# Kernel tuning notes

Measured on AMD Instinct MI355X. Metric: run time of the kernel, lower is better.

The kernel has to match this reference:

```python
import jax, jax.numpy as jnp
import numpy as np

B, S, L, H, E, V = 32, 48, 48, 1024, 1024, 32000


def setup_inputs() -> dict:
    key = jax.random.key(0)
    ks = jax.random.split(key, 16)
    s = 0.02
    return {
        "label": jax.random.randint(ks[0], (B, S), 0, V),
        "init_hidden": jax.random.normal(ks[1], (1, B, H), jnp.float32),
        "encoder_output": jax.random.normal(ks[2], (B, L, H), jnp.float32),
        "emb": jax.random.normal(ks[3], (V, E), jnp.float32) * s,
        "attn_W": jax.random.normal(ks[4], (2 * H, L), jnp.float32) * s,
        "attn_b": jnp.zeros((L,), jnp.float32),
        "comb_W": jax.random.normal(ks[5], (2 * H, H), jnp.float32) * s,
        "comb_b": jnp.zeros((H,), jnp.float32),
        "W_ih": jax.random.normal(ks[6], (E, 3 * H), jnp.float32) * s,
        "W_hh": jax.random.normal(ks[7], (H, 3 * H), jnp.float32) * s,
        "b_ih": jnp.zeros((3 * H,), jnp.float32),
        "b_hh": jnp.zeros((3 * H,), jnp.float32),
        "out_W": jax.random.normal(ks[8], (H, V), jnp.float32) * s,
        "out_b": jnp.zeros((V,), jnp.float32),
    }


def _decode(label, init_hidden, encoder_output, emb, attn_W, attn_b,
            comb_W, comb_b, W_ih, W_hh, b_ih, b_hh, out_W, out_b):
    # Teacher forcing (teaching_force_rate=1.0): inputs are relu(embedding(label[:, i]))
    xs = jax.nn.relu(emb[label])            # (B, S, E)
    xs = jnp.transpose(xs, (1, 0, 2))       # (S, B, E) for scan

    def step(h, xe):                        # h: (B,H), xe: (B,E)
        # Attention: Linear(cat(emb, hidden)) -> nn.Softmax() on a 3D (B,1,L)
        # tensor, which in torch defaults to dim=0 (the batch dim) -- replicated.
        sim = jnp.concatenate([xe, h], axis=-1) @ attn_W + attn_b   # (B, L)
        w = jax.nn.softmax(sim, axis=0)                             # over batch (faithful)
        ctx = jnp.einsum('bl,blh->bh', w, encoder_output)           # bmm
        g = jax.nn.relu(jnp.concatenate([ctx, xe], axis=-1) @ comb_W + comb_b)  # (B,H)
        # Single GRU step (torch gate order: r, z, n)
        gx = g @ W_ih + b_ih
        gh = h @ W_hh + b_hh
        xr, xz, xn = jnp.split(gx, 3, axis=-1)
        hr, hz, hn = jnp.split(gh, 3, axis=-1)
        r = jax.nn.sigmoid(xr + hr)
        z = jax.nn.sigmoid(xz + hz)
        n = jnp.tanh(xn + r * hn)
        h_new = (1.0 - z) * n + z * h
        out = jax.nn.log_softmax(h_new @ out_W + out_b, axis=-1)    # (B, V)
        return h_new, out

    _, outs = jax.lax.scan(step, init_hidden[0], xs)   # outs: (S, B, V)
    return jnp.transpose(outs, (1, 0, 2))              # (B, S, V)


def reference(label, init_hidden, encoder_output, emb, attn_W, attn_b,
              comb_W, comb_b, W_ih, W_hh, b_ih, b_hh, out_W, out_b):
    return _decode(label, init_hidden, encoder_output, emb, attn_W, attn_b,
                   comb_W, comb_b, W_ih, W_hh, b_ih, b_hh, out_W, out_b)
```

## Files before the change

### kernel.cpp

```cpp
#include <hip/hip_runtime.h>

#define NB 32
#define NS 48
#define NL 48
#define NH 1024
#define NE 1024
#define NV 32000
#define NR (NS*NB)
#define K3H 3072
#define RA_BLOCKS 64
#define RB_BLOCKS 128
#define RC_BLOCKS 64
#define NBLK_FULL (RA_BLOCKS + RB_BLOCKS + RC_BLOCKS)

typedef unsigned short u16;
typedef __bf16 bf16x8 __attribute__((ext_vector_type(8)));
typedef unsigned short ushort8 __attribute__((ext_vector_type(8)));
typedef float f32x4 __attribute__((ext_vector_type(4)));
typedef unsigned int uint4v __attribute__((ext_vector_type(4)));

__device__ __forceinline__ float bf2f(u16 x) {
    union { unsigned u; float f; } c; c.u = ((unsigned)x) << 16; return c.f;
}
__device__ __forceinline__ u16 f2bf(float f) {
// ... 29 lines not shown
    if ((prev & lineMask) == lineMask) {
        int p2 = __hip_atomic_fetch_add(superc, 1, __ATOMIC_RELAXED, __HIP_MEMORY_SCOPE_AGENT);
        if ((p2 & 7) == 7) {
#pragma unroll
            for (int i = 0; i < 24; ++i)
                asm volatile("global_store_dword %0, %1, off sc0 sc1"
                             :: "v"(bcast + i * 64), "v"(val) : "memory");
        }
    }
}

__global__ __launch_bounds__(256) void transpose_cast(const float* __restrict__ src, int K, int N,
                                                      char* __restrict__ dst, int bf16out) {
    __shared__ float tile[32][33];
    int k0 = blockIdx.y * 32, n0 = blockIdx.x * 32;
    int tx = threadIdx.x & 31, ty = threadIdx.x >> 5;
    for (int i = 0; i < 4; ++i) {
        int n = n0 + tx;
        float v = (n < N) ? src[(size_t)(k0 + ty + i*8) * N + n] : 0.f;
        tile[ty + i*8][tx] = v;
    }
    __syncthreads();
    for (int i = 0; i < 4; ++i) {
        int n = n0 + ty + i*8;
        int k = k0 + tx;
        if (n < N) {
            float v = tile[tx][ty + i*8];
            if (bf16out) ((u16*)dst)[(size_t)n * K + k] = f2bf(v);
            else         ((float*)dst)[(size_t)n * K + k] = v;
        }
    }
}

__global__ __launch_bounds__(256) void transpose_all(const float* __restrict__ Whh_, const float* __restrict__ Wih_,
                                                     const float* __restrict__ combW_, const float* __restrict__ attnW_,
                                                     u16* __restrict__ whht, u16* __restrict__ wiht,
                                                     u16* __restrict__ cw1t, u16* __restrict__ cw2t,
                                                     u16* __restrict__ aw2t, u16* __restrict__ aw1t) {
    __shared__ float tile[32][33];
    int bid = blockIdx.x;
    const float* src; u16* dst; int N, local;
    if (bid < 3072)      { src = Whh_;  dst = whht; N = 3072; local = bid; }
    else if (bid < 6144) { src = Wih_;  dst = wiht; N = 3072; local = bid - 3072; }
    else if (bid < 7168) { src = combW_; dst = cw1t; N = 1024; local = bid - 6144; }
    else if (bid < 8192) { src = combW_ + (size_t)NH * NH; dst = cw2t; N = 1024; local = bid - 7168; }
    else if (bid < 8256) { src = attnW_ + (size_t)NH * NL; dst = aw2t; N = 48; local = bid - 8192; }
    else                 { src = attnW_; dst = aw1t; N = 48; local = bid - 8256; }
    int tiles_x = (N + 31) >> 5;
    int n0 = (local % tiles_x) * 32, k0 = (local / tiles_x) * 32;
    int tx = threadIdx.x & 31, ty = threadIdx.x >> 5;
    for (int i = 0; i < 4; ++i) {
        int n = n0 + tx;
        float v = (n < N) ? src[(size_t)(k0 + ty + i*8) * N + n] : 0.f;
        tile[ty + i*8][tx] = v;
    }
    __syncthreads();
    for (int i = 0; i < 4; ++i) {
        int n = n0 + ty + i*8;
        int k = k0 + tx;
        if (n < N) dst[(size_t)n * 1024 + k] = f2bf(tile[tx][ty + i*8]);
    }
}

__global__ __launch_bounds__(256) void prep_inputs(const int* __restrict__ label, const float* __restrict__ emb,
                                                   const float* __restrict__ enc, const float* __restrict__ inith,
                                                   u16* __restrict__ xe, u16* __restrict__ encb, u16* __restrict__ hallx) {
    int blk = blockIdx.x, t = threadIdx.x;
    if (blk < NR) {
        int s = blk >> 5, b = blk & 31;
        int lab = label[b * NS + s];
        const float* src = emb + (size_t)lab * NE;
        u16* dst = xe + (size_t)blk * NE;
        for (int i = t; i < NE; i += 256) { float v = src[i]; dst[i] = f2bf(v > 0.f ? v : 0.f); }
    } else if (blk < 2 * NR) {
        int r = blk - NR;
        const float* src = enc + (size_t)r * NH;
        u16* dst = encb + (size_t)r * NH;
        for (int i = t; i < NH; i += 256) dst[i] = f2bf(src[i]);
    } else {
        int b = blk - 2 * NR;
        const float* src = inith + (size_t)b * NH;
        u16* dst = hallx + (size_t)b * NH;
        for (int i = t; i < NH; i += 256) dst[i] = f2bf(src[i]);
    }
}

__global__ __launch_bounds__(384) void simxe2_kernel(const u16* __restrict__ xe, const u16* __restrict__ aw1t,
                                                     const float* __restrict__ attnB, float* __restrict__ simxe) {
    int r = blockIdx.x, t = threadIdx.x;
    int l = t >> 3, part = t & 7;
    const u16* x = xe + (size_t)r * 1024 + part * 128;
    const u16* ww = aw1t + (size_t)l * 1024 + part * 128;
    float acc = 0.f;
#pragma unroll
    for (int k = 0; k < 128; k += 8) {
        ushort8 xv = *reinterpret_cast<const ushort8*>(x + k);
        ushort8 wv = *reinterpret_cast<const ushort8*>(ww + k);
#pragma unroll
        for (int u = 0; u < 8; ++u) acc += bf2f(xv[u]) * bf2f(wv[u]);
    }
    acc += __shfl_xor(acc, 1);
    acc += __shfl_xor(acc, 2);
    acc += __shfl_xor(acc, 4);
    if (part == 0) simxe[(size_t)r * NL + l] = acc + attnB[l];
}

template<int MODE>
__global__ __launch_bounds__(256) void gemm_bf16(const u16* __restrict__ A, const u16* __restrict__ Bt,
                                                 void* __restrict__ Cout, const float* __restrict__ bias, int N) {
    __shared__ u16 ldsA[128 * 64];
    __shared__ u16 ldsB[128 * 64];
    const int t = threadIdx.x;
    const int lane = t & 63, w = t >> 6;
    const int wm = w >> 1, wn = w & 1;
    const int m0 = blockIdx.x * 128, n0 = blockIdx.y * 128;
    f32x4 acc[4][4] = {};
    for (int kt = 0; kt < 16; ++kt) {
        const int k0 = kt * 64;
#pragma unroll
        for (int i = 0; i < 4; ++i) {
            int chunk = i * 256 + t;
            int row = chunk >> 3, slot = chunk & 7;
            int srck = ((slot ^ (row & 7)) * 8);
            gld_lds16(A  + (size_t)(m0 + row) * 1024 + k0 + srck, ldsA + (size_t)(i * 256 + w * 64) * 8);
            gld_lds16(Bt + (size_t)(n0 + row) * 1024 + k0 + srck, ldsB + (size_t)(i * 256 + w * 64) * 8);
        }
        asm volatile("s_waitcnt vmcnt(0)" ::: "memory");
        __syncthreads();
#pragma unroll
        for (int kk = 0; kk < 2; ++kk) {
            bf16x8 a[4], b[4];
#pragma unroll
            for (int f = 0; f < 4; ++f) {
                int rowA = wm * 64 + f * 16 + (lane & 15);
                int slotA = (kk * 4 + (lane >> 4)) ^ (rowA & 7);
                a[f] = *reinterpret_cast<const bf16x8*>(ldsA + rowA * 64 + slotA * 8);
                int rowB = wn * 64 + f * 16 + (lane & 15);
// ... 61 lines not shown
#pragma unroll
            for (int f = 0; f < 4; ++f) {
                int rowA = wm * 64 + f * 16 + (lane & 15);
                int slotA = (kk * 4 + (lane >> 4)) ^ (rowA & 7);
                a[f] = *reinterpret_cast<const bf16x8*>(ldsA + rowA * 64 + slotA * 8);
                int rowB = wn * 64 + f * 16 + (lane & 15);
                int slotB = (kk * 4 + (lane >> 4)) ^ (rowB & 7);
                b[f] = *reinterpret_cast<const bf16x8*>(ldsB + rowB * 64 + slotB * 8);
            }
#pragma unroll
            for (int fm = 0; fm < 4; ++fm)
#pragma unroll
                for (int fn = 0; fn < 4; ++fn)
                    acc[fm][fn] = mfma16(a[fm], b[fn], acc[fm][fn]);
        }
        __syncthreads();
    }
#pragma unroll
    for (int fm = 0; fm < 4; ++fm) {
#pragma unroll
        for (int fn = 0; fn < 4; ++fn) {
#pragma unroll
            for (int rr = 0; rr < 4; ++rr) {
                int m = m0 + wm * 64 + fm * 16 + (lane >> 4) * 4 + rr;
                int n = n0 + wn * 64 + fn * 16 + (lane & 15);
                float v = acc[fm][fn][rr];
                if (bias) v += bias[n];
                C[(size_t)m * NH + n] = f2bf(v);
            }
        }
    }
}

__device__ __forceinline__ void do_tile(char* smem, const u16* Ab, const u16* outWT,
                                        const float* outB, u16* logit,
                                        int mt, int nt, int t) {
    u16* ldsA = (u16*)smem;
    u16* ldsB = (u16*)(smem + 32768);
    const int w = t >> 6, lane = t & 63;
    const int r16 = lane & 15, kg = lane >> 4;
    const int wm = w >> 1, wn = w & 1;
    const int m0 = mt * 256, n0 = nt * 256;
    f32x4 acc[4][8] = {};
    for (int kt = 0; kt < 16; ++kt) {
        const int k0 = kt * 64;
#pragma unroll
        for (int i = 0; i < 4; ++i) {
            int chunk = i * 512 + t;
            int row = chunk >> 3, slot = chunk & 7;
            int srck = ((slot ^ (row & 7)) * 8);
            gld_lds16(Ab + (size_t)(m0 + row) * 1024 + k0 + srck,
                      ldsA + (size_t)(i * 512 + w * 64) * 8);
            gld_lds16(outWT + (size_t)(n0 + row) * 1024 + k0 + srck,
                      ldsB + (size_t)(i * 512 + w * 64) * 8);
        }
        asm volatile("s_waitcnt vmcnt(0)" ::: "memory");
        __syncthreads();
#pragma unroll
        for (int kk = 0; kk < 2; ++kk) {
            bf16x8 a[4], b[8];
#pragma unroll
            for (int f = 0; f < 4; ++f) {
                int rowA = wm * 64 + f * 16 + r16;
                int slotA = (kk * 4 + kg) ^ (rowA & 7);
                a[f] = *reinterpret_cast<const bf16x8*>(ldsA + rowA * 64 + slotA * 8);
            }
#pragma unroll
            for (int f = 0; f < 8; ++f) {
                int rowB = wn * 128 + f * 16 + r16;
                int slotB = (kk * 4 + kg) ^ (rowB & 7);
                b[f] = *reinterpret_cast<const bf16x8*>(ldsB + rowB * 64 + slotB * 8);
            }
#pragma unroll
            for (int fm = 0; fm < 4; ++fm)
#pragma unroll
                for (int fn = 0; fn < 8; ++fn)
                    acc[fm][fn] = mfma16(a[fm], b[fn], acc[fm][fn]);
        }
        __syncthreads();
    }
#pragma unroll
    for (int fm = 0; fm < 4; ++fm) {
#pragma unroll
        for (int fn = 0; fn < 8; ++fn) {
#pragma unroll
            for (int rr = 0; rr < 4; ++rr) {
                int m = m0 + wm * 64 + fm * 16 + kg * 4 + rr;
                int n = n0 + wn * 128 + fn * 16 + r16;
                float v = acc[fm][fn][rr] + outB[n];
                logit[((size_t)(m & 31) * NS + (m >> 5)) * NV + n] = f2bf(v);
            }
        }
    }
}

__device__ __forceinline__ void queue_gemm(char* smem, int* qslot, int* qcnt,
                                           const u16* Ab, const u16* outWT,
                                           const float* outB, u16* logit, int t) {
    for (;;) {
        __syncthreads();
        if (t == 0) *qslot = __hip_atomic_fetch_add(qcnt, 1, __ATOMIC_RELAXED, __HIP_MEMORY_SCOPE_AGENT);
        __syncthreads();
        int nt = *qslot;
        if (nt >= 125) return;
        do_tile(smem, Ab, outWT, outB, logit, 5, nt, t);
    }
}

__global__ __launch_bounds__(512) void recurrence10(
    const float* __restrict__ simxe, const u16* __restrict__ gxe,
    const u16* __restrict__ P, const u16* __restrict__ aw2t,
    const u16* __restrict__ whht, const u16* __restrict__ wiht,
    const float* __restrict__ b_ih, const float* __restrict__ b_hh,
    u16* __restrict__ g_rot, u16* __restrict__ hallx,
    const float* __restrict__ outW, const float* __restrict__ outB,
    u16* __restrict__ outWT, u16* __restrict__ logit, int* __restrict__ bar, int fused)
{
    __shared__ __align__(16) char smem[155776];
    int* cntA   = bar;
    int* cntB   = bar + 512;
    int* superA = bar + 1024;
    int* superB = bar + 1088;
    int* bcastA = bar + 1152;
    int* bcastB = bar + 2688;
    int* cntC   = bar + 4224;
    int* qcnt   = bar + 4288;
    int* qslot  = (int*)(smem + 153600);
    const int blk = blockIdx.x, t = threadIdx.x;
    const int lane = t & 63, w = t >> 6;
    const int r16 = lane & 15, kg = lane >> 4;
    const u16* Ab = hallx + NB * NH;

    if (blk < RA_BLOCKS) {
        int* myB = bcastB + (blk % 24) * 64;
        const int b = blk >> 1, half = blk & 1;
        u16*   W2T  = (u16*)smem;
        u16*   Pl   = (u16*)(smem + 99072);
        float* siml = (float*)(smem + 148224);
        float* wl   = (float*)(smem + 154496);
        u16*   gtmp = (u16*)(smem + 154752);
        for (int idx = t; idx < 48 * 1024; idx += 512) {
            int l = idx >> 10, k = idx & 1023;
            W2T[l * 1032 + k] = aw2t[idx];
        }
        for (int idx = t; idx < 48 * 512; idx += 512) {
            int l = idx >> 9, j = idx & 511;
            Pl[idx] = P[((size_t)(b * 48 + l)) * NH + half * 512 + j];
        }
        __syncthreads();
        const int mt = w & 1, nt = w >> 1;
        const int m0 = mt * 16, n0 = nt * 16;

        for (int s = 0; s < NS; ++s) {
            float gxev = bf2f(gxe[((size_t)(s * 32 + b)) * NH + half * 512 + t]);
            float sxv0 = 0.f, sxv1 = 0.f, sxv2 = 0.f, sxv3 = 0.f;
            if (w < 6) {
                const float* sxe = simxe + (size_t)(s * 32) * NL;
                sxv0 = sxe[(m0 + kg * 4 + 0) * NL + n0 + r16];
                sxv1 = sxe[(m0 + kg * 4 + 1) * NL + n0 + r16];
                sxv2 = sxe[(m0 + kg * 4 + 2) * NL + n0 + r16];
                sxv3 = sxe[(m0 + kg * 4 + 3) * NL + n0 + r16];
            }
            if (t == 0) waitb(myB, s);
            __syncthreads();
            const u16* hprev = hallx + (size_t)s * (NB * NH);
            if (w < 6) {
// ... 20 lines not shown
                float v2 = siml[(p * 4 + 2) * 49 + l];
                float v3 = siml[(p * 4 + 3) * 49 + l];
                float m = fmaxf(fmaxf(v0, v1), fmaxf(v2, v3));
                m = fmaxf(m, __shfl_xor(m, 1));
                m = fmaxf(m, __shfl_xor(m, 2));
                m = fmaxf(m, __shfl_xor(m, 4));
                float den = __expf(v0 - m) + __expf(v1 - m) + __expf(v2 - m) + __expf(v3 - m);
                den += __shfl_xor(den, 1);
                den += __shfl_xor(den, 2);
                den += __shfl_xor(den, 4);
                if (p == (b >> 2)) {
                    int bi = b & 3;
                    float vb = bi == 0 ? v0 : bi == 1 ? v1 : bi == 2 ? v2 : v3;
                    wl[l] = __expf(vb - m) / den;
                }
            }
            __syncthreads();
            {
                float acc = gxev;
#pragma unroll
                for (int l = 0; l < 48; ++l) acc += wl[l] * bf2f(Pl[l * 512 + t]);
                gtmp[t] = f2bf(fmaxf(acc, 0.f));
            }
            __syncthreads();
            if (t < 64) {
                uint4v v = *reinterpret_cast<const uint4v*>(gtmp + t * 8);
                st16_coh(g_rot + (size_t)s * (NB * NH) + (size_t)b * NH + half * 512 + t * 8, v);
            }
            if (t == 0) arrive2(cntA + (blk & 7) * 64, superA, bcastA, 7, s + 1);
        }
        if (fused) {
            if (t == 0) { waitb(myB, 48); waitb(cntC, RC_BLOCKS); }
            __syncthreads();
            queue_gemm(smem, qslot, qcnt, Ab, outWT, outB, logit, t);
        }
    } else if (blk < RA_BLOCKS + RB_BLOCKS) {
        const int rb = blk - RA_BLOCKS;
        int* myB = bcastB + (rb % 24) * 64;
        int* myA = bcastA + (rb % 24) * 64;
        const int c0 = rb * 8;
        u16*   Whh = (u16*)smem;
        u16*   Wih = (u16*)(smem + 66048);
        float* ghs = (float*)(smem + 132096);
        float* gxs = (float*)(smem + 140288);
        u16*   htmp = (u16*)(smem + 148480);
        for (int idx = t; idx < 32 * 1024; idx += 512) {
            int pr = idx >> 10, k = idx & 1023;
            u16 vh = 0, vi = 0;
            if (pr < 24) {
                size_t srow = (size_t)((pr >> 3) * 1024 + c0 + (pr & 7));
                vh = whht[srow * NH + k];
                vi = wiht[srow * NH + k];
            }
            Whh[pr * 1032 + k] = vh;
            Wih[pr * 1032 + k] = vi;
        }
        const int gb2 = (t & 255) >> 3, gcol = t & 7;
        const float bxr = b_ih[c0 + gcol], bxz = b_ih[1024 + c0 + gcol], bxn = b_ih[2048 + c0 + gcol];
        const float bhr = b_hh[c0 + gcol], bhz = b_hh[1024 + c0 + gcol], bhn = b_hh[2048 + c0 + gcol];
        __syncthreads();
        const int mt = (w >> 1) & 1, nt = w & 1, kh = w >> 2;
        const int m0 = mt * 16;

        for (int s = 0; s < NS; ++s) {
            if (t == 0) waitb(myB, s);
            __syncthreads();
            const u16* hprev = hallx + (size_t)s * (NB * NH);
// ... 25 lines not shown
                    acc0 = mfma16(*reinterpret_cast<const bf16x8*>(aP + k),
                                  *reinterpret_cast<const bf16x8*>(bP + k), acc0);
                    acc1 = mfma16(*reinterpret_cast<const bf16x8*>(aP + k + 32),
                                  *reinterpret_cast<const bf16x8*>(bP + k + 32), acc1);
                }
#pragma unroll
                for (int rr = 0; rr < 4; ++rr)
                    gxs[kh * 1024 + (m0 + kg * 4 + rr) * 32 + nt * 16 + r16] = acc0[rr] + acc1[rr];
            }
            __syncthreads();
            if (t < 256) {
                float gxr = gxs[gb2 * 32 + gcol]      + gxs[1024 + gb2 * 32 + gcol]      + bxr;
                float gxz = gxs[gb2 * 32 + 8 + gcol]  + gxs[1024 + gb2 * 32 + 8 + gcol]  + bxz;
                float gxn = gxs[gb2 * 32 + 16 + gcol] + gxs[1024 + gb2 * 32 + 16 + gcol] + bxn;
                float ghr = ghs[gb2 * 32 + gcol]      + ghs[1024 + gb2 * 32 + gcol]      + bhr;
                float ghz = ghs[gb2 * 32 + 8 + gcol]  + ghs[1024 + gb2 * 32 + 8 + gcol]  + bhz;
                float ghn = ghs[gb2 * 32 + 16 + gcol] + ghs[1024 + gb2 * 32 + 16 + gcol] + bhn;
                float rg = 1.f / (1.f + __expf(-(gxr + ghr)));
                float zg = 1.f / (1.f + __expf(-(gxz + ghz)));
                float ng = tanhf(gxn + rg * ghn);
                float hnew = (1.f - zg) * ng + zg * hold;
                htmp[t] = f2bf(hnew);
            }
            __syncthreads();
            if (t < 32) {
                uint4v v = *reinterpret_cast<const uint4v*>(htmp + t * 8);
                st16_coh(hallx + ((size_t)(s + 1) * NB + t) * NH + c0, v);
            }
            if (t == 0) arrive2(cntB + (rb & 7) * 64, superB, bcastB, 15, s + 1);
        }
        if (fused) {
            if (t == 0) { waitb(myB, 48); waitb(cntC, RC_BLOCKS); }
            __syncthreads();
            queue_gemm(smem, qslot, qcnt, Ab, outWT, outB, logit, t);
        }
    } else {
        const int rc = blk - (RA_BLOCKS + RB_BLOCKS);
        {
            float* ttile = (float*)smem;
            const int sub = t >> 7, u = t & 127;
            for (int T0 = 0; T0 < 32000; T0 += 256) {
                int T = T0 + rc * 4 + sub;
                int tn = T >> 5, tk = T & 31;
                int n0 = tn * 32, k0 = tk * 32;
                __syncthreads();
#pragma unroll
                for (int j = 0; j < 8; ++j) {
                    int e = j * 128 + u;
                    int row = e >> 5, col = e & 31;
                    ttile[(sub * 32 + row) * 33 + col] = outW[(size_t)(k0 + row) * NV + n0 + col];
                }
                __syncthreads();
                int nr = u >> 2, kc = u & 3;
                unsigned pk0, pk1, pk2, pk3;
                {
                    const float* base = ttile + (sub * 32 + kc * 8) * 33 + nr;
                    pk0 = (unsigned)f2bf(base[0])   | ((unsigned)f2bf(base[33])  << 16);
                    pk1 = (unsigned)f2bf(base[66])  | ((unsigned)f2bf(base[99])  << 16);
                    pk2 = (unsigned)f2bf(base[132]) | ((unsigned)f2bf(base[165]) << 16);
                    pk3 = (unsigned)f2bf(base[198]) | ((unsigned)f2bf(base[231]) << 16);
                }
                uint4v v; v[0] = pk0; v[1] = pk1; v[2] = pk2; v[3] = pk3;
                st16_coh(outWT + (size_t)(n0 + nr) * NH + k0 + kc * 8, v);
            }
            asm volatile("s_waitcnt vmcnt(0)" ::: "memory");
            __syncthreads();
            if (t == 0) {
                __hip_atomic_fetch_add(cntC, 1, __ATOMIC_RELAXED, __HIP_MEMORY_SCOPE_AGENT);
                waitb(cntC, RC_BLOCKS);
            }
            __syncthreads();
        }
        int lastReady = 0;
        for (int T = rc; T < 625; T += RC_BLOCKS) {
            int mt = T / 125, nt = T - mt * 125;
            int need = 8 * mt + 8;
            if (need > lastReady) {
                if (t == 0) waitb(bcastB + (rc % 24) * 64, need);
                lastReady = need;
            }
            __syncthreads();
            do_tile(smem, Ab, outWT, outB, logit, mt, nt, t);
        }
        if (t == 0) waitb(bcastB + (rc % 24) * 64, 48);
        __syncthreads();
        queue_gemm(smem, qslot, qcnt, Ab, outWT, outB, logit, t);
    }
}

__global__ __launch_bounds__(256) void logsoftmax_kernel(float* __restrict__ out) {
    __shared__ float red[8];
    float* row = out + (size_t)blockIdx.x * NV;
    int t = threadIdx.x;
    float m = -1e30f;
    for (int i = t; i < NV; i += 256) m = fmaxf(m, row[i]);
    for (int o = 32; o >= 1; o >>= 1) m = fmaxf(m, __shfl_xor(m, o));
    if ((t & 63) == 0) red[t >> 6] = m;
    __syncthreads();
    m = fmaxf(fmaxf(red[0], red[1]), fmaxf(red[2], red[3]));
    float sum = 0.f;
    for (int i = t; i < NV; i += 256) sum += __expf(row[i] - m);
    for (int o = 32; o >= 1; o >>= 1) sum += __shfl_xor(sum, o);
    if ((t & 63) == 0) red[4 + (t >> 6)] = sum;
    __syncthreads();
    sum = (red[4] + red[5]) + (red[6] + red[7]);
    float lse = m + __logf(sum);
    for (int i = t; i < NV; i += 256) row[i] = row[i] - lse;
}

__global__ __launch_bounds__(1024) void logsoftmax_bf16(const u16* __restrict__ lg, float* __restrict__ out) {
    __shared__ __align__(16) u16 rowb[NV];
    __shared__ float red[32];
    const u16* src = lg + (size_t)blockIdx.x * NV;
    float* dst = out + (size_t)blockIdx.x * NV;
    int t = threadIdx.x;
    for (int i = t; i < NV / 8; i += 1024)
        ((ushort8*)rowb)[i] = ((const ushort8*)src)[i];
    __syncthreads();
    float m = -1e30f;
    for (int i = t; i < NV; i += 1024) m = fmaxf(m, bf2f(rowb[i]));
    for (int o = 32; o >= 1; o >>= 1) m = fmaxf(m, __shfl_xor(m, o));
    if ((t & 63) == 0) red[t >> 6] = m;
    __syncthreads();
    m = red[0];
#pragma unroll
    for (int i = 1; i < 16; ++i) m = fmaxf(m, red[i]);
    float sum = 0.f;
    for (int i = t; i < NV; i += 1024) sum += __expf(bf2f(rowb[i]) - m);
    for (int o = 32; o >= 1; o >>= 1) sum += __shfl_xor(sum, o);
    if ((t & 63) == 0) red[16 + (t >> 6)] = sum;
    __syncthreads();
    sum = 0.f;
#pragma unroll
    for (int i = 0; i < 16; ++i) sum += red[16 + i];
    float lse = m + __logf(sum);
    for (int i = t; i < NV; i += 1024) dst[i] = bf2f(rowb[i]) - lse;
}

extern "C" void kernel_launch(void* const* d_in, const int* in_sizes, int n_in,
                              void* d_out, int out_size, void* d_ws, size_t ws_size,
                              hipStream_t stream) {
    const int*   label = (const int*)  d_in[0];
    const float* inith = (const float*)d_in[1];
    const float* enc   = (const float*)d_in[2];
    const float* emb   = (const float*)d_in[3];
    const float* attnW = (const float*)d_in[4];
    const float* attnB = (const float*)d_in[5];
    const float* combW = (const float*)d_in[6];
    const float* combB = (const float*)d_in[7];
    const float* Wih   = (const float*)d_in[8];
    const float* Whh   = (const float*)d_in[9];
    const float* bih   = (const float*)d_in[10];
    const float* bhh   = (const float*)d_in[11];
    const float* outW  = (const float*)d_in[12];
    const float* outB  = (const float*)d_in[13];
    char* ws = (char*)d_ws;

    size_t BAR_OFF    = 0;
    size_t OUTWT_OFF  = 32768;
    size_t WHHT_OFF   = OUTWT_OFF + (size_t)NV*NH*2;
    size_t WIHT_OFF   = WHHT_OFF + (size_t)K3H*NH*2;
    size_t CW1T_OFF   = WIHT_OFF + (size_t)K3H*NH*2;
    size_t CW2T_OFF   = CW1T_OFF + (size_t)NH*NH*2;
    size_t AW2T_OFF   = CW2T_OFF + (size_t)NH*NH*2;
    size_t AW1T_OFF   = AW2T_OFF + (size_t)NL*NH*2;
    size_t XE_OFF     = AW2T_OFF + (size_t)NL*NH*4;
    size_t ENCB_OFF   = XE_OFF   + (size_t)NR*NE*2;
    size_t SIMXE_OFF  = ENCB_OFF + (size_t)NR*NH*2;
    size_t GXE_OFF    = SIMXE_OFF+ (size_t)NR*NL*4;
    size_t P_OFF      = GXE_OFF  + (size_t)NR*NH*2;
    size_t HALL_OFF   = P_OFF    + (size_t)NR*NH*2;
    size_t GROT_OFF   = HALL_OFF + (size_t)(NS+1)*NB*NH*2;
    size_t LOGIT_OFF  = GROT_OFF + (size_t)NS*NB*NH*2;
    size_t TOTAL_NEED = LOGIT_OFF+ (size_t)NR*NV*2;

    int*   bar   = (int*)(ws + BAR_OFF);
    u16*   outWT = (u16*)(ws + OUTWT_OFF);
    u16*   whht  = (u16*)(ws + WHHT_OFF);
    u16*   wiht  = (u16*)(ws + WIHT_OFF);
    u16*   cw1t  = (u16*)(ws + CW1T_OFF);
    u16*   cw2t  = (u16*)(ws + CW2T_OFF);
    u16*   aw2t  = (u16*)(ws + AW2T_OFF);
    u16*   aw1t  = (u16*)(ws + AW1T_OFF);
    u16*   xe    = (u16*)(ws + XE_OFF);
    u16*   encb  = (u16*)(ws + ENCB_OFF);
    float* simxe = (float*)(ws + SIMXE_OFF);
    u16*   gxe   = (u16*)(ws + GXE_OFF);
    u16*   Pb    = (u16*)(ws + P_OFF);
    u16*   hallx = (u16*)(ws + HALL_OFF);
    u16*   grot  = (u16*)(ws + GROT_OFF);
    u16*   logit = (u16*)(ws + LOGIT_OFF);

    hipMemsetAsync(bar, 0, 32768, stream);
    prep_inputs<<<2 * NR + NB, 256, 0, stream>>>(label, emb, enc, inith, xe, encb, hallx);

    transpose_all<<<8320, 256, 0, stream>>>(Whh, Wih, combW, attnW,
                                            whht, wiht, cw1t, cw2t, aw2t, aw1t);

    simxe2_kernel<<<NR, 384, 0, stream>>>(xe, aw1t, attnB, simxe);
    gemm_pro<<<dim3(NR / 128, NH / 128, 2), 256, 0, stream>>>(xe, cw2t, encb, cw1t, gxe, Pb, combB);

    if (ws_size >= TOTAL_NEED) {
        recurrence10<<<NBLK_FULL, 512, 0, stream>>>(simxe, gxe, Pb, aw2t, whht, wiht,
                                                    bih, bhh, grot, hallx,
                                                    outW, outB, outWT, logit, bar, 1);
        logsoftmax_bf16<<<NR, 1024, 0, stream>>>(logit, (float*)d_out);
    } else {
        transpose_cast<<<dim3(NV / 32, 32), 256, 0, stream>>>(outW, NH, NV, (char*)outWT, 1);
        recurrence10<<<RA_BLOCKS + RB_BLOCKS, 512, 0, stream>>>(simxe, gxe, Pb, aw2t, whht, wiht,
                                                                bih, bhh, grot, hallx,
                                                                outW, outB, outWT, logit, bar, 0);
        gemm_bf16<1><<<dim3(NR / 128, NV / 128), 256, 0, stream>>>(hallx + (size_t)NB * NH, outWT, d_out, outB, NV);
        logsoftmax_kernel<<<NR, 256, 0, stream>>>((float*)d_out);
    }
}
```

Baseline: 900.7 us.

## Fuse log-softmax into persistent recurrence kernel and double-buffer output GEMM tiles

New measurement: 1.013 ms. 1.12x slower.

```diff
diff --git a/kernel.cpp b/kernel.cpp
--- a/kernel.cpp
+++ b/kernel.cpp
@@ -85,23 +85,50 @@
     }
 }
 
-__global__ __launch_bounds__(256) void transpose_all(const float* __restrict__ Whh_, const float* __restrict__ Wih_,
-                                                     const float* __restrict__ combW_, const float* __restrict__ attnW_,
-                                                     u16* __restrict__ whht, u16* __restrict__ wiht,
-                                                     u16* __restrict__ cw1t, u16* __restrict__ cw2t,
-                                                     u16* __restrict__ aw2t, u16* __restrict__ aw1t) {
+__global__ __launch_bounds__(256) void prologue_all(
+    const int* __restrict__ label, const float* __restrict__ emb,
+    const float* __restrict__ enc, const float* __restrict__ inith,
+    u16* __restrict__ xe, u16* __restrict__ encb, u16* __restrict__ hallx,
+    const float* __restrict__ Whh_, const float* __restrict__ Wih_,
+    const float* __restrict__ combW_, const float* __restrict__ attnW_,
+    u16* __restrict__ whht, u16* __restrict__ wiht,
+    u16* __restrict__ cw1t, u16* __restrict__ cw2t,
+    u16* __restrict__ aw2t, u16* __restrict__ aw1t)
+{
+    int bid = blockIdx.x, t = threadIdx.x;
+    if (bid < 3104) {
+        int blk = bid;
+        if (blk < NR) {
+            int s = blk >> 5, b = blk & 31;
+            int lab = label[b * NS + s];
+            const float* src = emb + (size_t)lab * NE;
+            u16* dst = xe + (size_t)blk * NE;
+            for (int i = t; i < NE; i += 256) { float v = src[i]; dst[i] = f2bf(v > 0.f ? v : 0.f); }
+        } else if (blk < 2 * NR) {
+            int r = blk - NR;
+            const float* src = enc + (size_t)r * NH;
+            u16* dst = encb + (size_t)r * NH;
+            for (int i = t; i < NH; i += 256) dst[i] = f2bf(src[i]);
+        } else {
+            int b = blk - 2 * NR;
+            const float* src = inith + (size_t)b * NH;
+            u16* dst = hallx + (size_t)b * NH;
+            for (int i = t; i < NH; i += 256) dst[i] = f2bf(src[i]);
+        }
+        return;
+    }
     __shared__ float tile[32][33];
-    int bid = blockIdx.x;
+    int tb = bid - 3104;
     const float* src; u16* dst; int N, local;
-    if (bid < 3072)      { src = Whh_;  dst = whht; N = 3072; local = bid; }
-    else if (bid < 6144) { src = Wih_;  dst = wiht; N = 3072; local = bid - 3072; }
-    else if (bid < 7168) { src = combW_; dst = cw1t; N = 1024; local = bid - 6144; }
-    else if (bid < 8192) { src = combW_ + (size_t)NH * NH; dst = cw2t; N = 1024; local = bid - 7168; }
-    else if (bid < 8256) { src = attnW_ + (size_t)NH * NL; dst = aw2t; N = 48; local = bid - 8192; }
-    else                 { src = attnW_; dst = aw1t; N = 48; local = bid - 8256; }
+    if (tb < 3072)      { src = Whh_;  dst = whht; N = 3072; local = tb; }
+    else if (tb < 6144) { src = Wih_;  dst = wiht; N = 3072; local = tb - 3072; }
+    else if (tb < 7168) { src = combW_; dst = cw1t; N = 1024; local = tb - 6144; }
+    else if (tb < 8192) { src = combW_ + (size_t)NH * NH; dst = cw2t; N = 1024; local = tb - 7168; }
+    else if (tb < 8256) { src = attnW_ + (size_t)NH * NL; dst = aw2t; N = 48; local = tb - 8192; }
+    else                { src = attnW_; dst = aw1t; N = 48; local = tb - 8256; }
     int tiles_x = (N + 31) >> 5;
     int n0 = (local % tiles_x) * 32, k0 = (local / tiles_x) * 32;
-    int tx = threadIdx.x & 31, ty = threadIdx.x >> 5;
+    int tx = t & 31, ty = t >> 5;
     for (int i = 0; i < 4; ++i) {
         int n = n0 + tx;
         float v = (n < N) ? src[(size_t)(k0 + ty + i*8) * N + n] : 0.f;
@@ -112,29 +139,6 @@
         int n = n0 + ty + i*8;
         int k = k0 + tx;
         if (n < N) dst[(size_t)n * 1024 + k] = f2bf(tile[tx][ty + i*8]);
-    }
-}
-
-__global__ __launch_bounds__(256) void prep_inputs(const int* __restrict__ label, const float* __restrict__ emb,
-                                                   const float* __restrict__ enc, const float* __restrict__ inith,
-                                                   u16* __restrict__ xe, u16* __restrict__ encb, u16* __restrict__ hallx) {
-    int blk = blockIdx.x, t = threadIdx.x;
-    if (blk < NR) {
-        int s = blk >> 5, b = blk & 31;
-        int lab = label[b * NS + s];
-        const float* src = emb + (size_t)lab * NE;
-        u16* dst = xe + (size_t)blk * NE;
-        for (int i = t; i < NE; i += 256) { float v = src[i]; dst[i] = f2bf(v > 0.f ? v : 0.f); }
-    } else if (blk < 2 * NR) {
-        int r = blk - NR;
-        const float* src = enc + (size_t)r * NH;
-        u16* dst = encb + (size_t)r * NH;
-        for (int i = t; i < NH; i += 256) dst[i] = f2bf(src[i]);
-    } else {
-        int b = blk - 2 * NR;
-        const float* src = inith + (size_t)b * NH;
-        u16* dst = hallx + (size_t)b * NH;
-        for (int i = t; i < NH; i += 256) dst[i] = f2bf(src[i]);
     }
 }
 
@@ -286,14 +290,15 @@
 __device__ __forceinline__ void do_tile(char* smem, const u16* Ab, const u16* outWT,
                                         const float* outB, u16* logit,
                                         int mt, int nt, int t) {
-    u16* ldsA = (u16*)smem;
-    u16* ldsB = (u16*)(smem + 32768);
+    u16* A0 = (u16*)smem;             u16* B0 = (u16*)(smem + 32768);
+    u16* A1 = (u16*)(smem + 65536);   u16* B1 = (u16*)(smem + 98304);
     const int w = t >> 6, lane = t & 63;
     const int r16 = lane & 15, kg = lane >> 4;
     const int wm = w >> 1, wn = w & 1;
     const int m0 = mt * 256, n0 = nt * 256;
     f32x4 acc[4][8] = {};
-    for (int kt = 0; kt < 16; ++kt) {
+
+    auto issue = [&](int kt, u16* la, u16* lb) {
         const int k0 = kt * 64;
 #pragma unroll
         for (int i = 0; i < 4; ++i) {
@@ -301,12 +306,12 @@
             int row = chunk >> 3, slot = chunk & 7;
             int srck = ((slot ^ (row & 7)) * 8);
             gld_lds16(Ab + (size_t)(m0 + row) * 1024 + k0 + srck,
-                      ldsA + (size_t)(i * 512 + w * 64) * 8);
+                      la + (size_t)(i * 512 + w * 64) * 8);
             gld_lds16(outWT + (size_t)(n0 + row) * 1024 + k0 + srck,
-                      ldsB + (size_t)(i * 512 + w * 64) * 8);
-        }
-        asm volatile("s_waitcnt vmcnt(0)" ::: "memory");
-        __syncthreads();
+                      lb + (size_t)(i * 512 + w * 64) * 8);
+        }
+    };
+    auto compute = [&](const u16* LA, const u16* LB) {
 #pragma unroll
         for (int kk = 0; kk < 2; ++kk) {
             bf16x8 a[4], b[8];
@@ -314,13 +319,13 @@
             for (int f = 0; f < 4; ++f) {
                 int rowA = wm * 64 + f * 16 + r16;
                 int slotA = (kk * 4 + kg) ^ (rowA & 7);
-                a[f] = *reinterpret_cast<const bf16x8*>(ldsA + rowA * 64 + slotA * 8);
+                a[f] = *reinterpret_cast<const bf16x8*>(LA + rowA * 64 + slotA * 8);
             }
 #pragma unroll
             for (int f = 0; f < 8; ++f) {
                 int rowB = wn * 128 + f * 16 + r16;
                 int slotB = (kk * 4 + kg) ^ (rowB & 7);
-                b[f] = *reinterpret_cast<const bf16x8*>(ldsB + rowB * 64 + slotB * 8);
+                b[f] = *reinterpret_cast<const bf16x8*>(LB + rowB * 64 + slotB * 8);
             }
 #pragma unroll
             for (int fm = 0; fm < 4; ++fm)
@@ -328,24 +333,84 @@
                 for (int fn = 0; fn < 8; ++fn)
                     acc[fm][fn] = mfma16(a[fm], b[fn], acc[fm][fn]);
         }
-        __syncthreads();
-    }
-#pragma unroll
-    for (int fm = 0; fm < 4; ++fm) {
-#pragma unroll
-        for (int fn = 0; fn < 8; ++fn) {
+    };
+
+    issue(0, A0, B0);
+    for (int kt = 0; kt < 16; kt += 2) {
+        issue(kt + 1, A1, B1);
+        asm volatile("s_waitcnt vmcnt(8)" ::: "memory");
+        __builtin_amdgcn_s_barrier();
+        compute(A0, B0);
+        __builtin_amdgcn_s_barrier();
+        if (kt + 2 < 16) {
+            issue(kt + 2, A0, B0);
+            asm volatile("s_waitcnt vmcnt(8)" ::: "memory");
+        } else {
+            asm volatile("s_waitcnt vmcnt(0)" ::: "memory");
+        }
+        __builtin_amdgcn_s_barrier();
+        compute(A1, B1);
+        __builtin_amdgcn_s_barrier();
+    }
+    u16* stg = (u16*)smem;
+#pragma unroll
+    for (int fm = 0; fm < 4; ++fm)
+#pragma unroll
+        for (int fn = 0; fn < 8; ++fn)
 #pragma unroll
             for (int rr = 0; rr < 4; ++rr) {
-                int m = m0 + wm * 64 + fm * 16 + kg * 4 + rr;
-                int n = n0 + wn * 128 + fn * 16 + r16;
-                float v = acc[fm][fn][rr] + outB[n];
-                logit[((size_t)(m & 31) * NS + (m >> 5)) * NV + n] = f2bf(v);
-            }
-        }
-    }
-}
-
-__device__ __forceinline__ void queue_gemm(char* smem, int* qslot, int* qcnt,
+                int mr = wm * 64 + fm * 16 + kg * 4 + rr;
+                int nc = wn * 128 + fn * 16 + r16;
+                stg[mr * 264 + nc] = f2bf(acc[fm][fn][rr] + outB[n0 + nc]);
+            }
+    __syncthreads();
+    {
+        int mr = t >> 1, cb = (t & 1) * 128;
+        int m = m0 + mr;
+        int orow = (m & 31) * NS + (m >> 5);
+        u16* dst = logit + (size_t)orow * NV + n0 + cb;
+        const u16* srcr = stg + mr * 264 + cb;
+#pragma unroll
+        for (int i = 0; i < 16; ++i) {
+            uint4v v = *reinterpret_cast<const uint4v*>(srcr + i * 8);
+            st16_coh(dst + i * 8, v);
+        }
+    }
+    asm volatile("s_waitcnt vmcnt(0)" ::: "memory");
+    __syncthreads();
+}
+
+__device__ __forceinline__ void softmax_row(char* smem, const u16* logit, float* dout, int m, int t) {
+    u16* rowb = (u16*)smem;
+    float* red = (float*)(smem + 64000);
+    const int orow = (m & 31) * NS + (m >> 5);
+    const u16* src = logit + (size_t)orow * NV;
+    float* dst = dout + (size_t)orow * NV;
+    for (int i = t; i < NV / 8; i += 512)
+        ((ushort8*)rowb)[i] = ((const ushort8*)src)[i];
+    __syncthreads();
+    float mx = -1e30f;
+    for (int i = t; i < NV; i += 512) mx = fmaxf(mx, bf2f(rowb[i]));
+    for (int o = 32; o >= 1; o >>= 1) mx = fmaxf(mx, __shfl_xor(mx, o));
+    if ((t & 63) == 0) red[t >> 6] = mx;
+    __syncthreads();
+    mx = red[0];
+#pragma unroll
+    for (int i = 1; i < 8; ++i) mx = fmaxf(mx, red[i]);
+    float sum = 0.f;
+    for (int i = t; i < NV; i += 512) sum += __expf(bf2f(rowb[i]) - mx);
+    for (int o = 32; o >= 1; o >>= 1) sum += __shfl_xor(sum, o);
+    if ((t & 63) == 0) red[8 + (t >> 6)] = sum;
+    __syncthreads();
+    sum = 0.f;
+#pragma unroll
+    for (int i = 0; i < 8; ++i) sum += red[8 + i];
+    float lse = mx + __logf(sum);
+    for (int i = t; i < NV; i += 512) dst[i] = bf2f(rowb[i]) - lse;
+    __syncthreads();
+}
+
+__device__ __forceinline__ void queue_gemm(char* smem, int* qslot, int* qcnt, int* gd5,
                                            const u16* Ab, const u16* outWT,
                                            const float* outB, u16* logit, int t) {
     for (;;) {
@@ -355,17 +420,35 @@
         int nt = *qslot;
         if (nt >= 125) return;
         do_tile(smem, Ab, outWT, outB, logit, 5, nt, t);
-    }
-}
-
-__global__ __launch_bounds__(512) void recurrence10(
+        if (t == 0) __hip_atomic_fetch_add(gd5, 1, __ATOMIC_RELAXED, __HIP_MEMORY_SCOPE_AGENT);
+    }
+}
+
+__device__ __forceinline__ void drain_softmax(char* smem, int* qslot, int* gd, int* rowq,
+                                              const u16* logit, float* dout, int t) {
+    for (int g = 0; g < 6; ++g) {
+        if (t == 0) waitb(gd + g * 64, 125);
+        __syncthreads();
+        for (;;) {
+            __syncthreads();
+            if (t == 0) *qslot = __hip_atomic_fetch_add(rowq + g * 64, 1, __ATOMIC_RELAXED, __HIP_MEMORY_SCOPE_AGENT);
+            __syncthreads();
+            int q = *qslot;
+            if (q >= 256) break;
+            softmax_row(smem, logit, dout, g * 256 + q, t);
+        }
+    }
+}
+
+__global__ __launch_bounds__(512) void recurrence11(
     const float* __restrict__ simxe, const u16* __restrict__ gxe,
     const u16* __restrict__ P, const u16* __restrict__ aw2t,
     const u16* __restrict__ whht, const u16* __restrict__ wiht,
     const float* __restrict__ b_ih, const float* __restrict__ b_hh,
     u16* __restrict__ g_rot, u16* __restrict__ hallx,
     const float* __restrict__ outW, const float* __restrict__ outB,
-    u16* __restrict__ outWT, u16* __restrict__ logit, int* __restrict__ bar, int fused)
+    u16* __restrict__ outWT, u16* __restrict__ logit, float* __restrict__ dout,
+    int* __restrict__ bar, int fused)
 {
     __shared__ __align__(16) char smem[155776];
     int* cntA   = bar;
@@ -376,6 +459,8 @@
     int* bcastB = bar + 2688;
     int* cntC   = bar + 4224;
     int* qcnt   = bar + 4288;
+    int* gd     = bar + 4352;
+    int* rowq   = bar + 4736;
     int* qslot  = (int*)(smem + 153600);
     const int blk = blockIdx.x, t = threadIdx.x;
     const int lane = t & 63, w = t >> 6;
@@ -469,7 +554,8 @@
         if (fused) {
             if (t == 0) { waitb(myB, 48); waitb(cntC, RC_BLOCKS); }
             __syncthreads();
-            queue_gemm(smem, qslot, qcnt, Ab, outWT, outB, logit, t);
+            queue_gemm(smem, qslot, qcnt, gd + 5 * 64, Ab, outWT, outB, logit, t);
+            drain_softmax(smem, qslot, gd, rowq, logit, dout, t);
         }
     } else if (blk < RA_BLOCKS + RB_BLOCKS) {
         const int rb = blk - RA_BLOCKS;
@@ -561,7 +647,8 @@
         if (fused) {
             if (t == 0) { waitb(myB, 48); waitb(cntC, RC_BLOCKS); }
             __syncthreads();
-            queue_gemm(smem, qslot, qcnt, Ab, outWT, outB, logit, t);
+            queue_gemm(smem, qslot, qcnt, gd + 5 * 64, Ab, outWT, outB, logit, t);
+            drain_softmax(smem, qslot, gd, rowq, logit, dout, t);
         }
     } else {
         const int rc = blk - (RA_BLOCKS + RB_BLOCKS);
@@ -600,20 +687,28 @@
             }
             __syncthreads();
         }
-        int lastReady = 0;
-        for (int T = rc; T < 625; T += RC_BLOCKS) {
-            int mt = T / 125, nt = T - mt * 125;
-            int need = 8 * mt + 8;
-            if (need > lastReady) {
-                if (t == 0) waitb(bcastB + (rc % 24) * 64, need);
-                lastReady = need;
-            }
-            __syncthreads();
-            do_tile(smem, Ab, outWT, outB, logit, mt, nt, t);
+        for (int g = 0; g < 5; ++g) {
+            if (t == 0) waitb(bcastB + (rc % 24) * 64, 8 * g + 8);
+            __syncthreads();
+            for (int T = rc; T < 125; T += RC_BLOCKS) {
+                do_tile(smem, Ab, outWT, outB, logit, g, T, t);
+                if (t == 0) __hip_atomic_fetch_add(gd + g * 64, 1, __ATOMIC_RELAXED, __HIP_MEMORY_SCOPE_AGENT);
+            }
+            if (t == 0) waitb(gd + g * 64, 125);
+            __syncthreads();
+            for (;;) {
+                __syncthreads();
+                if (t == 0) *qslot = __hip_atomic_fetch_add(rowq + g * 64, 1, __ATOMIC_RELAXED, __HIP_MEMORY_SCOPE_AGENT);
+                __syncthreads();
+                int q = *qslot;
+                if (q >= 256) break;
+                softmax_row(smem, logit, dout, g * 256 + q, t);
+            }
         }
         if (t == 0) waitb(bcastB + (rc % 24) * 64, 48);
         __syncthreads();
-        queue_gemm(smem, qslot, qcnt, Ab, outWT, outB, logit, t);
+        queue_gemm(smem, qslot, qcnt, gd + 5 * 64, Ab, outWT, outB, logit, t);
+        drain_softmax(smem, qslot, gd, rowq, logit, dout, t);
     }
 }
 
@@ -635,35 +730,6 @@
     sum = (red[4] + red[5]) + (red[6] + red[7]);
     float lse = m + __logf(sum);
     for (int i = t; i < NV; i += 256) row[i] = row[i] - lse;
-}
-
-__global__ __launch_bounds__(1024) void logsoftmax_bf16(const u16* __restrict__ lg, float* __restrict__ out) {
-    __shared__ __align__(16) u16 rowb[NV];
-    __shared__ float red[32];
-    const u16* src = lg + (size_t)blockIdx.x * NV;
-    float* dst = out + (size_t)blockIdx.x * NV;
-    int t = threadIdx.x;
-    for (int i = t; i < NV / 8; i += 1024)
-        ((ushort8*)rowb)[i] = ((const ushort8*)src)[i];
-    __syncthreads();
-    float m = -1e30f;
-    for (int i = t; i < NV; i += 1024) m = fmaxf(m, bf2f(rowb[i]));
-    for (int o = 32; o >= 1; o >>= 1) m = fmaxf(m, __shfl_xor(m, o));
-    if ((t & 63) == 0) red[t >> 6] = m;
-    __syncthreads();
-    m = red[0];
-#pragma unroll
-    for (int i = 1; i < 16; ++i) m = fmaxf(m, red[i]);
-    float sum = 0.f;
-    for (int i = t; i < NV; i += 1024) sum += __expf(bf2f(rowb[i]) - m);
-    for (int o = 32; o >= 1; o >>= 1) sum += __shfl_xor(sum, o);
-    if ((t & 63) == 0) red[16 + (t >> 6)] = sum;
-    __syncthreads();
-    sum = 0.f;
-#pragma unroll
-    for (int i = 0; i < 16; ++i) sum += red[16 + i];
-    float lse = m + __logf(sum);
-    for (int i = t; i < NV; i += 1024) dst[i] = bf2f(rowb[i]) - lse;
 }
 
 extern "C" void kernel_launch(void* const* d_in, const int* in_sizes, int n_in,
@@ -721,24 +787,22 @@
     u16*   logit = (u16*)(ws + LOGIT_OFF);
 
     hipMemsetAsync(bar, 0, 32768, stream);
-    prep_inputs<<<2 * NR + NB, 256, 0, stream>>>(label, emb, enc, inith, xe, encb, hallx);
-
-    transpose_all<<<8320, 256, 0, stream>>>(Whh, Wih, combW, attnW,
-                                            whht, wiht, cw1t, cw2t, aw2t, aw1t);
+    prologue_all<<<3104 + 8320, 256, 0, stream>>>(label, emb, enc, inith, xe, encb, hallx,
+                                                  Whh, Wih, combW, attnW,
+                                                  whht, wiht, cw1t, cw2t, aw2t, aw1t);
 
     simxe2_kernel<<<NR, 384, 0, stream>>>(xe, aw1t, attnB, simxe);
     gemm_pro<<<dim3(NR / 128, NH / 128, 2), 256, 0, stream>>>(xe, cw2t, encb, cw1t, gxe, Pb, combB);
 
     if (ws_size >= TOTAL_NEED) {
-        recurrence10<<<NBLK_FULL, 512, 0, stream>>>(simxe, gxe, Pb, aw2t, whht, wiht,
+        recurrence11<<<NBLK_FULL, 512, 0, stream>>>(simxe, gxe, Pb, aw2t, whht, wiht,
                                                     bih, bhh, grot, hallx,
-                                                    outW, outB, outWT, logit, bar, 1);
-        logsoftmax_bf16<<<NR, 1024, 0, stream>>>(logit, (float*)d_out);
+                                                    outW, outB, outWT, logit, (float*)d_out, bar, 1);
     } else {
         transpose_cast<<<dim3(NV / 32, 32), 256, 0, stream>>>(outW, NH, NV, (char*)outWT, 1);
-        recurrence10<<<RA_BLOCKS + RB_BLOCKS, 512, 0, stream>>>(simxe, gxe, Pb, aw2t, whht, wiht,
+        recurrence11<<<RA_BLOCKS + RB_BLOCKS, 512, 0, stream>>>(simxe, gxe, Pb, aw2t, whht, wiht,
                                                                 bih, bhh, grot, hallx,
-                                                                outW, outB, outWT, logit, bar, 0);
+                                                                outW, outB, outWT, logit, (float*)d_out, bar, 0);
         gemm_bf16<1><<<dim3(NR / 128, NV / 128), 256, 0, stream>>>(hallx + (size_t)NB * NH, outWT, d_out, outB, NV);
         logsoftmax_kernel<<<NR, 256, 0, stream>>>((float*)d_out);
     }
```

## Fuse prologue kernels and move projection GEMMs into persistent recurrence kernel

Applied to the files above, without the earlier changes.

Measured after the change: 956.1 us. 6.1% more time.

```diff
diff --git a/kernel.cpp b/kernel.cpp
--- a/kernel.cpp
+++ b/kernel.cpp
@@ -85,23 +85,70 @@
     }
 }
 
-__global__ __launch_bounds__(256) void transpose_all(const float* __restrict__ Whh_, const float* __restrict__ Wih_,
-                                                     const float* __restrict__ combW_, const float* __restrict__ attnW_,
-                                                     u16* __restrict__ whht, u16* __restrict__ wiht,
-                                                     u16* __restrict__ cw1t, u16* __restrict__ cw2t,
-                                                     u16* __restrict__ aw2t, u16* __restrict__ aw1t) {
+__global__ __launch_bounds__(256) void prologue_all(
+    const int* __restrict__ label, const float* __restrict__ emb,
+    const float* __restrict__ enc, const float* __restrict__ inith,
+    u16* __restrict__ xe, u16* __restrict__ encb, u16* __restrict__ hallx,
+    const float* __restrict__ Whh_, const float* __restrict__ Wih_,
+    const float* __restrict__ combW_, const float* __restrict__ attnW_,
+    const float* __restrict__ attnB_, float* __restrict__ simxe,
+    u16* __restrict__ whht, u16* __restrict__ wiht,
+    u16* __restrict__ cw1t, u16* __restrict__ cw2t,
+    u16* __restrict__ aw2t, u16* __restrict__ aw1t)
+{
+    int bid = blockIdx.x, t = threadIdx.x;
+    if (bid >= 11424) {
+        int r = bid - 11424;
+        int s = r >> 5, b = r & 31;
+        int lab = label[b * NS + s];
+        const float* x = emb + (size_t)lab * NE;
+        int l = t >> 2, part = t & 3;
+        if (l < 48) {
+            float acc = 0.f;
+            for (int k = part * 256; k < part * 256 + 256; ++k) {
+                float v = x[k];
+                v = v > 0.f ? v : 0.f;
+                acc += v * attnW_[(size_t)k * NL + l];
+            }
+            acc += __shfl_xor(acc, 1);
+            acc += __shfl_xor(acc, 2);
+            if (part == 0) simxe[(size_t)r * NL + l] = acc + attnB_[l];
+        }
+        return;
+    }
+    if (bid < 3104) {
+        int blk = bid;
+        if (blk < NR) {
+            int s = blk >> 5, b = blk & 31;
+            int lab = label[b * NS + s];
+            const float* src = emb + (size_t)lab * NE;
+            u16* dst = xe + (size_t)blk * NE;
+            for (int i = t; i < NE; i += 256) { float v = src[i]; dst[i] = f2bf(v > 0.f ? v : 0.f); }
+        } else if (blk < 2 * NR) {
+            int r = blk - NR;
+            const float* src = enc + (size_t)r * NH;
+            u16* dst = encb + (size_t)r * NH;
+            for (int i = t; i < NH; i += 256) dst[i] = f2bf(src[i]);
+        } else {
+            int b = blk - 2 * NR;
+            const float* src = inith + (size_t)b * NH;
+            u16* dst = hallx + (size_t)b * NH;
+            for (int i = t; i < NH; i += 256) dst[i] = f2bf(src[i]);
+        }
+        return;
+    }
     __shared__ float tile[32][33];
-    int bid = blockIdx.x;
+    int tb = bid - 3104;
     const float* src; u16* dst; int N, local;
-    if (bid < 3072)      { src = Whh_;  dst = whht; N = 3072; local = bid; }
-    else if (bid < 6144) { src = Wih_;  dst = wiht; N = 3072; local = bid - 3072; }
-    else if (bid < 7168) { src = combW_; dst = cw1t; N = 1024; local = bid - 6144; }
-    else if (bid < 8192) { src = combW_ + (size_t)NH * NH; dst = cw2t; N = 1024; local = bid - 7168; }
-    else if (bid < 8256) { src = attnW_ + (size_t)NH * NL; dst = aw2t; N = 48; local = bid - 8192; }
-    else                 { src = attnW_; dst = aw1t; N = 48; local = bid - 8256; }
+    if (tb < 3072)      { src = Whh_;  dst = whht; N = 3072; local = tb; }
+    else if (tb < 6144) { src = Wih_;  dst = wiht; N = 3072; local = tb - 3072; }
+    else if (tb < 7168) { src = combW_; dst = cw1t; N = 1024; local = tb - 6144; }
+    else if (tb < 8192) { src = combW_ + (size_t)NH * NH; dst = cw2t; N = 1024; local = tb - 7168; }
+    else if (tb < 8256) { src = attnW_ + (size_t)NH * NL; dst = aw2t; N = 48; local = tb - 8192; }
+    else                { src = attnW_; dst = aw1t; N = 48; local = tb - 8256; }
     int tiles_x = (N + 31) >> 5;
     int n0 = (local % tiles_x) * 32, k0 = (local / tiles_x) * 32;
-    int tx = threadIdx.x & 31, ty = threadIdx.x >> 5;
+    int tx = t & 31, ty = t >> 5;
     for (int i = 0; i < 4; ++i) {
         int n = n0 + tx;
         float v = (n < N) ? src[(size_t)(k0 + ty + i*8) * N + n] : 0.f;
@@ -113,49 +160,6 @@
         int k = k0 + tx;
         if (n < N) dst[(size_t)n * 1024 + k] = f2bf(tile[tx][ty + i*8]);
     }
-}
-
-__global__ __launch_bounds__(256) void prep_inputs(const int* __restrict__ label, const float* __restrict__ emb,
-                                                   const float* __restrict__ enc, const float* __restrict__ inith,
-                                                   u16* __restrict__ xe, u16* __restrict__ encb, u16* __restrict__ hallx) {
-    int blk = blockIdx.x, t = threadIdx.x;
-    if (blk < NR) {
-        int s = blk >> 5, b = blk & 31;
-        int lab = label[b * NS + s];
-        const float* src = emb + (size_t)lab * NE;
-        u16* dst = xe + (size_t)blk * NE;
-        for (int i = t; i < NE; i += 256) { float v = src[i]; dst[i] = f2bf(v > 0.f ? v : 0.f); }
-    } else if (blk < 2 * NR) {
-        int r = blk - NR;
-        const float* src = enc + (size_t)r * NH;
-        u16* dst = encb + (size_t)r * NH;
-        for (int i = t; i < NH; i += 256) dst[i] = f2bf(src[i]);
-    } else {
-        int b = blk - 2 * NR;
-        const float* src = inith + (size_t)b * NH;
-        u16* dst = hallx + (size_t)b * NH;
-        for (int i = t; i < NH; i += 256) dst[i] = f2bf(src[i]);
-    }
-}
-
-__global__ __launch_bounds__(384) void simxe2_kernel(const u16* __restrict__ xe, const u16* __restrict__ aw1t,
-                                                     const float* __restrict__ attnB, float* __restrict__ simxe) {
-    int r = blockIdx.x, t = threadIdx.x;
-    int l = t >> 3, part = t & 7;
-    const u16* x = xe + (size_t)r * 1024 + part * 128;
-    const u16* ww = aw1t + (size_t)l * 1024 + part * 128;
-    float acc = 0.f;
-#pragma unroll
-    for (int k = 0; k < 128; k += 8) {
-        ushort8 xv = *reinterpret_cast<const ushort8*>(x + k);
-        ushort8 wv = *reinterpret_cast<const ushort8*>(ww + k);
-#pragma unroll
-        for (int u = 0; u < 8; ++u) acc += bf2f(xv[u]) * bf2f(wv[u]);
-    }
-    acc += __shfl_xor(acc, 1);
-    acc += __shfl_xor(acc, 2);
-    acc += __shfl_xor(acc, 4);
-    if (part == 0) simxe[(size_t)r * NL + l] = acc + attnB[l];
 }
 
 template<int MODE>
@@ -283,6 +287,73 @@
     }
 }
 
+__device__ __forceinline__ void pre_gemm_tile(char* smem, const u16* A, const u16* Bt,
+                                              u16* C, const float* bias, int m0, int n0, int t) {
+    u16* ldsA = (u16*)smem;
+    u16* ldsB = (u16*)(smem + 16384);
+    const int w = t >> 6, lane = t & 63;
+    const int r16 = lane & 15, kg = lane >> 4;
+    const int wm = w >> 2, wn = w & 3;
+    f32x4 acc[4][2] = {};
+    for (int kt = 0; kt < 16; ++kt) {
+        const int k0 = kt * 64;
+#pragma unroll
+        for (int i = 0; i < 2; ++i) {
+            int chunk = i * 512 + t;
+            int row = chunk >> 3, slot = chunk & 7;
+            int srck = ((slot ^ (row & 7)) * 8);
+            gld_lds16(A  + (size_t)(m0 + row) * 1024 + k0 + srck, ldsA + (size_t)(i * 512 + w * 64) * 8);
+            gld_lds16(Bt + (size_t)(n0 + row) * 1024 + k0 + srck, ldsB + (size_t)(i * 512 + w * 64) * 8);
+        }
+        asm volatile("s_waitcnt vmcnt(0)" ::: "memory");
+        __syncthreads();
+#pragma unroll
+        for (int kk = 0; kk < 2; ++kk) {
+            bf16x8 a[4], b[2];
+#pragma unroll
+            for (int f = 0; f < 4; ++f) {
+                int rowA = wm * 64 + f * 16 + r16;
+                int slotA = (kk * 4 + kg) ^ (rowA & 7);
+                a[f] = *reinterpret_cast<const bf16x8*>(ldsA + rowA * 64 + slotA * 8);
+            }
+#pragma unroll
+            for (int f = 0; f < 2; ++f) {
+                int rowB = wn * 32 + f * 16 + r16;
+                int slotB = (kk * 4 + kg) ^ (rowB & 7);
+                b[f] = *reinterpret_cast<const bf16x8*>(ldsB + rowB * 64 + slotB * 8);
+            }
+#pragma unroll
+            for (int fm = 0; fm < 4; ++fm)
+#pragma unroll
+                for (int fn = 0; fn < 2; ++fn)
+                    acc[fm][fn] = mfma16(a[fm], b[fn], acc[fm][fn]);
+        }
+        __syncthreads();
+    }
+    u16* stg = (u16*)smem;
+#pragma unroll
+    for (int fm = 0; fm < 4; ++fm)
+#pragma unroll
+        for (int fn = 0; fn < 2; ++fn)
+#pragma unroll
+            for (int rr = 0; rr < 4; ++rr) {
+                int mr = wm * 64 + fm * 16 + kg * 4 + rr;
+                int nc = wn * 32 + fn * 16 + r16;
+                float v = acc[fm][fn][rr];
+                if (bias) v += bias[n0 + nc];
+                stg[mr * 136 + nc] = f2bf(v);
+            }
+    __syncthreads();
+#pragma unroll
+    for (int i = 0; i < 4; ++i) {
+        int vidx = t * 4 + i;
+        int row = vidx >> 4, cv = vidx & 15;
+        uint4v v = *reinterpret_cast<const uint4v*>(stg + row * 136 + cv * 8);
+        st16_coh(C + (size_t)(m0 + row) * NH + n0 + cv * 8, v);
+    }
+    __syncthreads();
+}
+
 __device__ __forceinline__ void do_tile(char* smem, const u16* Ab, const u16* outWT,
                                         const float* outB, u16* logit,
                                         int mt, int nt, int t) {
@@ -358,14 +429,19 @@
     }
 }
 
-__global__ __launch_bounds__(512) void recurrence10(
+__global__ __launch_bounds__(512) void recurrence12(
     const float* __restrict__ simxe, const u16* __restrict__ gxe,
     const u16* __restrict__ P, const u16* __restrict__ aw2t,
     const u16* __restrict__ whht, const u16* __restrict__ wiht,
     const float* __restrict__ b_ih, const float* __restrict__ b_hh,
     u16* __restrict__ g_rot, u16* __restrict__ hallx,
     const float* __restrict__ outW, const float* __restrict__ outB,
-    u16* __restrict__ outWT, u16* __restrict__ logit, int* __restrict__ bar, int fused)
+    u16* __restrict__ outWT, u16* __restrict__ logit,
+    const u16* __restrict__ xe, const u16* __restrict__ encb,
+    const u16* __restrict__ cw1t, const u16* __restrict__ cw2t,
+    const float* __restrict__ combB,
+    u16* __restrict__ gxe_w, u16* __restrict__ Pb_w,
+    int* __restrict__ bar, int fused)
 {
     __shared__ __align__(16) char smem[155776];
     int* cntA   = bar;
@@ -376,13 +452,32 @@
     int* bcastB = bar + 2688;
     int* cntC   = bar + 4224;
     int* qcnt   = bar + 4288;
+    int* cntP   = bar + 4352;
     int* qslot  = (int*)(smem + 153600);
     const int blk = blockIdx.x, t = threadIdx.x;
     const int lane = t & 63, w = t >> 6;
     const int r16 = lane & 15, kg = lane >> 4;
     const u16* Ab = hallx + NB * NH;
 
+    if (fused && blk < 192) {
+        int z = blk / 96, local = blk % 96;
+        int pmt = local >> 3, pnt = local & 7;
+        const u16* A  = z ? encb : xe;
+        const u16* Bt = z ? cw1t : cw2t;
+        u16* C        = z ? Pb_w : gxe_w;
+        pre_gemm_tile(smem, A, Bt, C, z ? nullptr : combB, pmt * 128, pnt * 128, t);
+        if (t == 0) {
+            asm volatile("s_waitcnt vmcnt(0)" ::: "memory");
+            __hip_atomic_fetch_add(cntP, 1, __ATOMIC_RELAXED, __HIP_MEMORY_SCOPE_AGENT);
+        }
+        __syncthreads();
+    }
+
     if (blk < RA_BLOCKS) {
+        if (fused) {
+            if (t == 0) waitb(cntP, 192);
+            __syncthreads();
+        }
         int* myB = bcastB + (blk % 24) * 64;
         const int b = blk >> 1, half = blk & 1;
         u16*   W2T  = (u16*)smem;
@@ -721,24 +816,25 @@
     u16*   logit = (u16*)(ws + LOGIT_OFF);
 
     hipMemsetAsync(bar, 0, 32768, stream);
-    prep_inputs<<<2 * NR + NB, 256, 0, stream>>>(label, emb, enc, inith, xe, encb, hallx);
-
-    transpose_all<<<8320, 256, 0, stream>>>(Whh, Wih, combW, attnW,
-                                            whht, wiht, cw1t, cw2t, aw2t, aw1t);
-
-    simxe2_kernel<<<NR, 384, 0, stream>>>(xe, aw1t, attnB, simxe);
-    gemm_pro<<<dim3(NR / 128, NH / 128, 2), 256, 0, stream>>>(xe, cw2t, encb, cw1t, gxe, Pb, combB);
+    prologue_all<<<3104 + 8320 + NR, 256, 0, stream>>>(label, emb, enc, inith, xe, encb, hallx,
+                                                       Whh, Wih, combW, attnW, attnB, simxe,
+                                                       whht, wiht, cw1t, cw2t, aw2t, aw1t);
 
     if (ws_size >= TOTAL_NEED) {
-        recurrence10<<<NBLK_FULL, 512, 0, stream>>>(simxe, gxe, Pb, aw2t, whht, wiht,
+        recurrence12<<<NBLK_FULL, 512, 0, stream>>>(simxe, gxe, Pb, aw2t, whht, wiht,
                                                     bih, bhh, grot, hallx,
-                                                    outW, outB, outWT, logit, bar, 1);
+                                                    outW, outB, outWT, logit,
+                                                    xe, encb, cw1t, cw2t, combB, gxe, Pb,
+                                                    bar, 1);
         logsoftmax_bf16<<<NR, 1024, 0, stream>>>(logit, (float*)d_out);
     } else {
+        gemm_pro<<<dim3(NR / 128, NH / 128, 2), 256, 0, stream>>>(xe, cw2t, encb, cw1t, gxe, Pb, combB);
         transpose_cast<<<dim3(NV / 32, 32), 256, 0, stream>>>(outW, NH, NV, (char*)outWT, 1);
-        recurrence10<<<RA_BLOCKS + RB_BLOCKS, 512, 0, stream>>>(simxe, gxe, Pb, aw2t, whht, wiht,
+        recurrence12<<<RA_BLOCKS + RB_BLOCKS, 512, 0, stream>>>(simxe, gxe, Pb, aw2t, whht, wiht,
                                                                 bih, bhh, grot, hallx,
-                                                                outW, outB, outWT, logit, bar, 0);
+                                                                outW, outB, outWT, logit,
+                                                                xe, encb, cw1t, cw2t, combB, gxe, Pb,
+                                                                bar, 0);
         gemm_bf16<1><<<dim3(NR / 128, NV / 128), 256, 0, stream>>>(hallx + (size_t)NB * NH, outWT, d_out, outB, NV);
         logsoftmax_kernel<<<NR, 256, 0, stream>>>((float*)d_out);
     }
```
